# Optimization experiments

Measured on AMD Instinct MI355X. Metric: run time of the kernel, lower is better.

## Reference

```python
import jax, jax.numpy as jnp
import numpy as np

B, L, D, H, TOPO = 2, 1024, 1024, 16, 8
Dh = D // H
N_SLOTS = B * L


def _rope_apply(x, cos, sin):
    # x: [B,H,L,Dh]; cos/sin: [B,1,L,Dh//2]
    x1 = x[..., 0::2]
    x2 = x[..., 1::2]
    y1 = x1 * cos - x2 * sin
    y2 = x1 * sin + x2 * cos
    return jnp.stack([y1, y2], axis=-1).reshape(x.shape)


def setup_inputs() -> dict:
    key = jax.random.key(0)
    ks = jax.random.split(key, 6)
    x = jax.random.normal(ks[0], (B, L, D), dtype=jnp.float32)
    topo_active = jax.random.normal(ks[1], (B, L, TOPO), dtype=jnp.float32)
    k_cache = jnp.zeros((1, H, N_SLOTS, Dh), dtype=jnp.float32)
    v_cache = jnp.zeros((1, H, N_SLOTS, Dh), dtype=jnp.float32)
    Wqkv = jax.random.normal(ks[2], (3 * D, D), dtype=jnp.float32) * 0.02
    Wproj = jax.random.normal(ks[3], (D, D), dtype=jnp.float32) * 0.02
    Wfreq = jax.random.normal(ks[4], (Dh // 2, TOPO), dtype=jnp.float32) * 0.02
    # each token (b, pos) writes to physical slot b*L + pos
    slot_mapping = jnp.arange(N_SLOTS, dtype=jnp.int64)
    # paged causal mask: query (b, i) may see slot s iff slot belongs to batch b and pos(s) <= i
    s = jnp.arange(N_SLOTS)
    sb = s // L           # batch owning each slot
    sp = s % L            # position within that sequence
    b_idx = jnp.arange(B)[:, None, None]
    i_idx = jnp.arange(L)[None, :, None]
    block_mask = ((sb[None, None, :] == b_idx) & (sp[None, None, :] <= i_idx))[:, None]  # [B,1,L,S]
    return {"x": x, "topo_active": topo_active, "k_cache": k_cache, "v_cache": v_cache,
            "Wqkv": Wqkv, "Wproj": Wproj, "Wfreq": Wfreq,
            "slot_mapping": slot_mapping, "block_mask": block_mask}


def reference(x, topo_active, k_cache, v_cache, Wqkv, Wproj, Wfreq, slot_mapping, block_mask):
    Bx, Lx, Dx = x.shape
    # qkv projection -> q,k,v [B,H,L,Dh]
    qkv = (x @ Wqkv.T).reshape(Bx, Lx, 3, H, Dh).transpose(2, 0, 3, 1, 4)
    q, k, v = qkv[0], qkv[1], qkv[2]
    # RnRoPE: topo -> per-position frequencies, rotate q and k
    freqs = (topo_active @ Wfreq.T)[:, None]  # [B,1,L,Dh//2]
    cos, sin = jnp.cos(freqs), jnp.sin(freqs)
    q = _rope_apply(q, cos, sin)
    k = _rope_apply(k, cos, sin)
    # commit new k/v into the paged cache via slot_mapping scatter
    k_flat = k.transpose(0, 2, 1, 3).reshape(Bx * Lx, H, Dh).swapaxes(0, 1)  # [H,BL,Dh]
    v_flat = v.transpose(0, 2, 1, 3).reshape(Bx * Lx, H, Dh).swapaxes(0, 1)
    kc = k_cache[0].at[:, slot_mapping].set(k_flat)  # [H,S,Dh]
    vc = v_cache[0].at[:, slot_mapping].set(v_flat)
    # masked (block-sparse) attention over the physical cache
    scale = 1.0 / jnp.sqrt(jnp.float32(Dh))
    scores = jnp.einsum('bhld,hsd->bhls', q, kc) * scale
    scores = jnp.where(block_mask, scores, -jnp.inf)
    p = jax.nn.softmax(scores, axis=-1)
    out = jnp.einsum('bhls,hsd->bhld', p, vc)
    out = out.transpose(0, 2, 1, 3).reshape(Bx, Lx, Dx)
    return out @ Wproj.T
```

## Files before the change

kernel.cpp:

```cpp
#include <hip/hip_runtime.h>
#include <hip/hip_bf16.h>
#include <math.h>

#define H_N 16
#define DH 64
#define LSEQ 1024
#define BATCH 2
#define NSLOT 2048
#define DMODEL 1024

typedef __bf16 bf16x8 __attribute__((ext_vector_type(8)));
typedef __bf16 bf16x4 __attribute__((ext_vector_type(4)));
typedef float f32x4 __attribute__((ext_vector_type(4)));

__global__ __launch_bounds__(256) void k_setup(const float* __restrict__ x,
                                               const float* __restrict__ Wqkv,
                                               const float* __restrict__ Wproj,
                                               const float* __restrict__ topo,
                                               const float* __restrict__ Wfreq,
                                               __bf16* __restrict__ xb,
                                               __bf16* __restrict__ Wqkvb,
                                               __bf16* __restrict__ Wprojb,
                                               float* __restrict__ cosb,
                                               float* __restrict__ sinb) {
    int blk = blockIdx.x;
    if (blk < 6144) {
        const float* in;
        __bf16* out;
        int base;
        if (blk < 2048)      { in = x;     out = xb;     base = blk; }
        else if (blk < 5120) { in = Wqkv;  out = Wqkvb;  base = blk - 2048; }
        else                 { in = Wproj; out = Wprojb; base = blk - 5120; }
        int i = (base * 256 + threadIdx.x) * 4;
        float4 v = *reinterpret_cast<const float4*>(in + i);
        struct B4 { __bf16 a, b, c, d; };
        B4 o{(__bf16)v.x, (__bf16)v.y, (__bf16)v.z, (__bf16)v.w};
        *reinterpret_cast<B4*>(out + i) = o;
    } else {
        int s = (blk - 6144) * 8 + (threadIdx.x >> 5);
        int j = threadIdx.x & 31;
        float f = 0.f;
#pragma unroll
        for (int t = 0; t < 8; ++t) f += topo[s * 8 + t] * Wfreq[j * 8 + t];
        cosb[s * 32 + j] = cosf(f);
        sinb[s * 32 + j] = sinf(f);
    }
}

template <int BM, int BN, int BK>
__device__ __forceinline__ void gemm_coreT(const __bf16* __restrict__ A,
                                           const __bf16* __restrict__ Bm,
                                           int K, int m0, int n0,
                                           __bf16* As, __bf16* Bs,
                                           f32x4 acc[BM / 32][BN / 32],
                                           int tid, int wr, int wc, int lane) {
    constexpr int MF = BM / 32, NF = BN / 32;
    constexpr int SLOTS = BK / 8;
    constexpr int RPI = 256 / SLOTS;
    constexpr int AIT = BM / RPI;
    constexpr int BIT = BN / RPI;
    const f32x4 z = {0.f, 0.f, 0.f, 0.f};
#pragma unroll
    for (int m = 0; m < MF; ++m)
#pragma unroll
        for (int n = 0; n < NF; ++n) acc[m][n] = z;

    const int l15 = lane & 15, g = lane >> 4;
    const int wv = tid >> 6;
    const int srow = tid / SLOTS, sslot = tid % SLOTS;
    const int ssrc = (sslot ^ (srow & 7)) * 8;

#pragma unroll
    for (int i = 0; i < AIT; ++i) {
        int row = i * RPI + srow;
        __builtin_amdgcn_global_load_lds(
            (const __attribute__((address_space(1))) void*)(A + (size_t)(m0 + row) * K + ssrc),
            (__attribute__((address_space(3))) void*)(As + i * 2048 + wv * 512), 16, 0, 0);
    }
#pragma unroll
    for (int i = 0; i < BIT; ++i) {
        int row = i * RPI + srow;
        __builtin_amdgcn_global_load_lds(
            (const __attribute__((address_space(1))) void*)(Bm + (size_t)(n0 + row) * K + ssrc),
            (__attribute__((address_space(3))) void*)(Bs + i * 2048 + wv * 512), 16, 0, 0);
    }
    __syncthreads();

    const int NT = K / BK;
    for (int t = 0; t < NT; ++t) {
        const int cur = t & 1;
        __bf16* Ac = As + cur * (BM * BK);
        __bf16* Bc = Bs + cur * (BN * BK);
        if (t + 1 < NT) {
            const int k0 = (t + 1) * BK;
            __bf16* An = As + (1 - cur) * (BM * BK);
            __bf16* Bn = Bs + (1 - cur) * (BN * BK);
#pragma unroll
            for (int i = 0; i < AIT; ++i) {
                int row = i * RPI + srow;
                __builtin_amdgcn_global_load_lds(
                    (const __attribute__((address_space(1))) void*)(A + (size_t)(m0 + row) * K + k0 + ssrc),
                    (__attribute__((address_space(3))) void*)(An + i * 2048 + wv * 512), 16, 0, 0);
            }
#pragma unroll
            for (int i = 0; i < BIT; ++i) {
                int row = i * RPI + srow;
                __builtin_amdgcn_global_load_lds(
                    (const __attribute__((address_space(1))) void*)(Bm + (size_t)(n0 + row) * K + k0 + ssrc),
                    (__attribute__((address_space(3))) void*)(Bn + i * 2048 + wv * 512), 16, 0, 0);
            }
        }
        __builtin_amdgcn_s_setprio(1);
#pragma unroll
        for (int kk = 0; kk < BK / 32; ++kk) {
            const int k16 = kk * 4 + g;
            bf16x8 af[MF], bfr[NF];
#pragma unroll
            for (int m = 0; m < MF; ++m) {
                int row = wr * (BM / 2) + m * 16 + l15;
                int slot = k16 ^ (row & 7);
                af[m] = *reinterpret_cast<const bf16x8*>(Ac + row * BK + slot * 8);
            }
#pragma unroll
            for (int n = 0; n < NF; ++n) {
                int col = wc * (BN / 2) + n * 16 + l15;
                int slot = k16 ^ (col & 7);
                bfr[n] = *reinterpret_cast<const bf16x8*>(Bc + col * BK + slot * 8);
            }
#pragma unroll
            for (int m = 0; m < MF; ++m)
#pragma unroll
                for (int n = 0; n < NF; ++n)
                    acc[m][n] = __builtin_amdgcn_mfma_f32_16x16x32_bf16(af[m], bfr[n], acc[m][n], 0, 0, 0);
        }
        __builtin_amdgcn_s_setprio(0);
        __syncthreads();
    }
}

__global__ __launch_bounds__(256, 2) void k_qkv_mfma(const __bf16* __restrict__ xb,
                                                     const __bf16* __restrict__ Wb,
                                                     const float* __restrict__ cosb,
                                                     const float* __restrict__ sinb,
                                                     __bf16* __restrict__ Qb,
                                                     __bf16* __restrict__ Kb,
                                                     __bf16* __restrict__ Vtb) {
    __shared__ __bf16 As[2][128 * 64];
    __shared__ __bf16 Bs[2][96 * 64];
    int lin = blockIdx.x;
    int newlin = (lin & 7) * 64 + (lin >> 3);
    const int m0 = (newlin & 15) * 128, n0 = (newlin >> 4) * 96;
    const int tid = threadIdx.x, lane = tid & 63, w = tid >> 6;
    const int wr = w >> 1, wc = w & 1;
    const int l15 = lane & 15, g = lane >> 4;
    f32x4 acc[4][3];
    gemm_coreT<128, 96, 64>(xb, Wb, DMODEL, m0, n0, &As[0][0], &Bs[0][0], acc, tid, wr, wc, lane);

    const int rbase = m0 + wr * 64;
#pragma unroll
    for (int n = 0; n < 3; ++n) {
        int c = n0 + wc * 48 + n * 16 + l15;
        int part = c >> 10, h = (c >> 6) & 15, d = c & 63, jj = d >> 1;
#pragma unroll
        for (int m = 0; m < 4; ++m) {
            int sbase = rbase + m * 16 + g * 4;
            if (part < 2) {
                __bf16* dst = (part == 0) ? Qb : Kb;
#pragma unroll
                for (int j = 0; j < 4; ++j) {
                    int s = sbase + j;
                    float v = acc[m][n][j];
                    float partner = __shfl_xor(v, 1);
                    float cs = cosb[s * 32 + jj], sn = sinb[s * 32 + jj];
                    float outv = (d & 1) ? fmaf(v, cs, partner * sn) : fmaf(v, cs, -partner * sn);
                    dst[((size_t)h * NSLOT + s) * DH + d] = (__bf16)outv;
                }
            } else {
                bf16x4 pk;
#pragma unroll
                for (int j = 0; j < 4; ++j) pk[j] = (__bf16)acc[m][n][j];
                *reinterpret_cast<bf16x4*>(&Vtb[((size_t)h * DH + d) * NSLOT + sbase]) = pk;
            }
        }
    }
}

__global__ __launch_bounds__(256, 2) void k_attn9(const __bf16* __restrict__ Qg,
                                                  const __bf16* __restrict__ Kg,
                                                  const __bf16* __restrict__ Vt,
                                                  __bf16* __restrict__ AO) {
    int lin = blockIdx.x + 16 * (blockIdx.y + 16 * blockIdx.z);
    const int x = lin & 7;
    const int t = lin >> 3;
    const int b = x >> 2;
    const int h = (x & 3) * 4 + (t & 3);
    const int v = t >> 2;
    const int bx = (v < 8) ? v : 23 - v;

    const int tid = threadIdx.x, w = tid >> 6, lane = tid & 63;
    const int l15 = lane & 15, g = lane >> 4;
    const int q0 = bx * 64 + w * 16;

    __shared__ __bf16 Ks[2][128 * 64];
    __shared__ __bf16 Vs[2][64 * 128];
    __shared__ __bf16 P_lds[4][16 * 128];

    const __bf16* Qh = Qg + ((size_t)h * NSLOT + b * LSEQ) * DH;
    const __bf16* Kh = Kg + ((size_t)h * NSLOT + b * LSEQ) * DH;
    const __bf16* Vh = Vt + ((size_t)h * DH) * NSLOT + b * LSEQ;

    bf16x8 qf[2];
#pragma unroll
    for (int g2 = 0; g2 < 2; ++g2)
        qf[g2] = *reinterpret_cast<const bf16x8*>(Qh + (size_t)(q0 + l15) * DH + g2 * 32 + g * 8);

    const f32x4 z = {0.f, 0.f, 0.f, 0.f};
    f32x4 ao[4];
#pragma unroll
    for (int dt = 0; dt < 4; ++dt) ao[dt] = z;
    float lsum[4] = {0.f, 0.f, 0.f, 0.f};

    const int nch = (bx >> 1) + 1;

#pragma unroll
    for (int i = 0; i < 4; ++i) {
        int u = i * 256 + tid;
        {
            int row = u >> 3, slot = u & 7, srcs = (slot ^ (row & 7)) * 8;
            __builtin_amdgcn_global_load_lds(
                (const __attribute__((address_space(1))) void*)(Kh + (size_t)row * DH + srcs),
                (__attribute__((address_space(3))) void*)(&Ks[0][i * 2048 + (tid >> 6) * 512]), 16, 0, 0);
        }
        {
            int row = u >> 4, slot = u & 15, srcs = (slot ^ (row & 7)) * 8;
            __builtin_amdgcn_global_load_lds(
                (const __attribute__((address_space(1))) void*)(Vh + (size_t)row * NSLOT + srcs),
                (__attribute__((address_space(3))) void*)(&Vs[0][i * 2048 + (tid >> 6) * 512]), 16, 0, 0);
        }
    }
    __syncthreads();

    for (int ch = 0; ch < nch; ++ch) {
        const int cur = ch & 1;
        if (ch + 1 < nch) {
            const int nsp = (ch + 1) * 128;
#pragma unroll
            for (int i = 0; i < 4; ++i) {
                int u = i * 256 + tid;
                {
                    int row = u >> 3, slot = u & 7, srcs = (slot ^ (row & 7)) * 8;
                    __builtin_amdgcn_global_load_lds(
                        (const __attribute__((address_space(1))) void*)(Kh + (size_t)(nsp + row) * DH + srcs),
                        (__attribute__((address_space(3))) void*)(&Ks[1 - cur][i * 2048 + (tid >> 6) * 512]), 16, 0, 0);
                }
                {
                    int row = u >> 4, slot = u & 15, srcs = (slot ^ (row & 7)) * 8;
                    __builtin_amdgcn_global_load_lds(
                        (const __attribute__((address_space(1))) void*)(Vh + (size_t)row * NSLOT + nsp + srcs),
                        (__attribute__((address_space(3))) void*)(&Vs[1 - cur][i * 2048 + (tid >> 6) * 512]), 16, 0, 0);
                }
            }
        }

        f32x4 s[8];
#pragma unroll
        for (int n = 0; n < 8; ++n) s[n] = z;
        __builtin_amdgcn_s_setprio(1);
#pragma unroll
        for (int g2 = 0; g2 < 2; ++g2) {
#pragma unroll
            for (int n = 0; n < 8; ++n) {
                int r = n * 16 + l15;
                int slot = ((g2 << 2) + g) ^ (r & 7);
                bf16x8 kf = *reinterpret_cast<const bf16x8*>(&Ks[cur][r * 64 + slot * 8]);
                s[n] = __builtin_amdgcn_mfma_f32_16x16x32_bf16(qf[g2], kf, s[n], 0, 0, 0);
            }
        }
        __builtin_amdgcn_s_setprio(0);

        const bool last = (ch == nch - 1);
        const int sp0 = ch * 128;
#pragma unroll
        for (int n = 0; n < 8; ++n) {
            int key = sp0 + n * 16 + l15;
#pragma unroll
            for (int j = 0; j < 4; ++j) {
                float sc = s[n][j] * 0.125f;
                if (last && key > q0 + g * 4 + j) sc = -INFINITY;
                float p = __expf(sc);
                s[n][j] = p;
                lsum[j] += p;
            }
        }

#pragma unroll
        for (int j = 0; j < 4; ++j) {
            int row = g * 4 + j;
#pragma unroll
            for (int n = 0; n < 8; ++n) {
                int slot = n * 2 + (l15 >> 3);
                P_lds[w][row * 128 + ((slot ^ (row & 7)) << 3) + (l15 & 7)] = (__bf16)s[n][j];
            }
        }

        bf16x8 pf[4];
#pragma unroll
        for (int kb = 0; kb < 4; ++kb)
            pf[kb] = *reinterpret_cast<const bf16x8*>(
                &P_lds[w][l15 * 128 + (((kb << 2) + g) ^ (l15 & 7)) * 8]);

        __builtin_amdgcn_s_setprio(1);
#pragma unroll
        for (int kb = 0; kb < 4; ++kb) {
#pragma unroll
            for (int dt = 0; dt < 4; ++dt) {
                int rv = dt * 16 + l15;
                int slot = ((kb << 2) + g) ^ (rv & 7);
                bf16x8 vf = *reinterpret_cast<const bf16x8*>(&Vs[cur][rv * 128 + slot * 8]);
                ao[dt] = __builtin_amdgcn_mfma_f32_16x16x32_bf16(pf[kb], vf, ao[dt], 0, 0, 0);
            }
        }
        __builtin_amdgcn_s_setprio(0);

        __syncthreads();
    }

    float lrow[4];
#pragma unroll
    for (int j = 0; j < 4; ++j) {
        float vv = lsum[j];
#pragma unroll
        for (int off = 1; off < 16; off <<= 1) vv += __shfl_xor(vv, off);
        lrow[j] = vv;
    }

#pragma unroll
    for (int dt = 0; dt < 4; ++dt)
#pragma unroll
        for (int j = 0; j < 4; ++j) {
            int q = q0 + g * 4 + j;
            AO[(size_t)(b * LSEQ + q) * DMODEL + h * 64 + dt * 16 + l15] =
                (__bf16)(ao[dt][j] / lrow[j]);
        }
}

__global__ __launch_bounds__(256, 2) void k_proj_mfma(const __bf16* __restrict__ AO,
                                                      const __bf16* __restrict__ Wb,
                                                      float* __restrict__ out) {
    __shared__ __bf16 As[2][64 * 128];
    __shared__ __bf16 Bs[2][64 * 128];
    int lin = blockIdx.x;
    int newlin = (lin & 7) * 64 + (lin >> 3);
    const int m0 = (newlin & 31) * 64, n0 = (newlin >> 5) * 64;
    const int tid = threadIdx.x, lane = tid & 63, w = tid >> 6;
    const int wr = w >> 1, wc = w & 1;
    const int l15 = lane & 15, g = lane >> 4;
    f32x4 acc[2][2];
    gemm_coreT<64, 64, 128>(AO, Wb, DMODEL, m0, n0, &As[0][0], &Bs[0][0], acc, tid, wr, wc, lane);

#pragma unroll
    for (int n = 0; n < 2; ++n) {
        int c = n0 + wc * 32 + n * 16 + l15;
#pragma unroll
        for (int m = 0; m < 2; ++m) {
#pragma unroll
            for (int j = 0; j < 4; ++j) {
                int s = m0 + wr * 32 + m * 16 + g * 4 + j;
                out[(size_t)s * DMODEL + c] = acc[m][n][j];
            }
        }
    }
}

extern "C" void kernel_launch(void* const* d_in, const int* in_sizes, int n_in,
                              void* d_out, int out_size, void* d_ws, size_t ws_size,
                              hipStream_t stream) {
    const float* x     = (const float*)d_in[0];
    const float* topo  = (const float*)d_in[1];
    const float* Wqkv  = (const float*)d_in[4];
    const float* Wproj = (const float*)d_in[5];
    const float* Wfreq = (const float*)d_in[6];
    float* out = (float*)d_out;

    char* wsb = (char*)d_ws;
    __bf16* xb     = (__bf16*)(wsb + 0);
    __bf16* Wqkvb  = (__bf16*)(wsb + (4u << 20));
    __bf16* Wprojb = (__bf16*)(wsb + (10u << 20));
    float*  cosb   = (float*)(wsb + (12u << 20));
    float*  sinb   = (float*)(wsb + (12u << 20) + 262144);
    __bf16* Qb     = (__bf16*)(wsb + (12u << 20) + 524288);
    __bf16* Kb     = (__bf16*)(wsb + (16u << 20) + 524288);
    __bf16* Vtb    = (__bf16*)(wsb + (20u << 20) + 524288);
    __bf16* AO     = (__bf16*)(wsb + (24u << 20) + 524288);

    hipLaunchKernelGGL(k_setup, dim3(6400), dim3(256), 0, stream,
                       x, Wqkv, Wproj, topo, Wfreq, xb, Wqkvb, Wprojb, cosb, sinb);
    hipLaunchKernelGGL(k_qkv_mfma, dim3(512), dim3(256), 0, stream,
                       xb, Wqkvb, cosb, sinb, Qb, Kb, Vtb);
    hipLaunchKernelGGL(k_attn9, dim3(LSEQ / 64, H_N, BATCH), dim3(256), 0, stream,
                       Qb, Kb, Vtb, AO);
    hipLaunchKernelGGL(k_proj_mfma, dim3(512), dim3(256), 0, stream,
                       AO, Wprojb, out);
}
```

Measured before the change: 62.54 us.

## Fuse all four stages into one cooperative persistent kernel with grid syncs

Merges the setup, QKV GEMM with RoPE, attention and projection kernels into a single cooperative kernel of 512 blocks, separated by grid-wide syncs. The goal is to remove the launch gaps and tail effects between the four separate launches. The fused attention phase loses double-buffered K/V prefetch and now loads each chunk synchronously, which adds memory latency. Grid syncs and a single fixed 64KB shared-memory allocation may also limit occupancy; the old multi-kernel path is kept as a fallback.

```diff
diff --git a/kernel.cpp b/kernel.cpp
--- a/kernel.cpp
+++ b/kernel.cpp
@@ -1,6 +1,9 @@
 #include <hip/hip_runtime.h>
 #include <hip/hip_bf16.h>
+#include <hip/hip_cooperative_groups.h>
 #include <math.h>
+
+namespace cg = cooperative_groups;
 
 #define H_N 16
 #define DH 64
@@ -12,40 +15,6 @@
 typedef __bf16 bf16x8 __attribute__((ext_vector_type(8)));
 typedef __bf16 bf16x4 __attribute__((ext_vector_type(4)));
 typedef float f32x4 __attribute__((ext_vector_type(4)));
-
-__global__ __launch_bounds__(256) void k_setup(const float* __restrict__ x,
-                                               const float* __restrict__ Wqkv,
-                                               const float* __restrict__ Wproj,
-                                               const float* __restrict__ topo,
-                                               const float* __restrict__ Wfreq,
-                                               __bf16* __restrict__ xb,
-                                               __bf16* __restrict__ Wqkvb,
-                                               __bf16* __restrict__ Wprojb,
-                                               float* __restrict__ cosb,
-                                               float* __restrict__ sinb) {
-    int blk = blockIdx.x;
-    if (blk < 6144) {
-        const float* in;
-        __bf16* out;
-        int base;
-        if (blk < 2048)      { in = x;     out = xb;     base = blk; }
-        else if (blk < 5120) { in = Wqkv;  out = Wqkvb;  base = blk - 2048; }
-        else                 { in = Wproj; out = Wprojb; base = blk - 5120; }
-        int i = (base * 256 + threadIdx.x) * 4;
-        float4 v = *reinterpret_cast<const float4*>(in + i);
-        struct B4 { __bf16 a, b, c, d; };
-        B4 o{(__bf16)v.x, (__bf16)v.y, (__bf16)v.z, (__bf16)v.w};
-        *reinterpret_cast<B4*>(out + i) = o;
-    } else {
-        int s = (blk - 6144) * 8 + (threadIdx.x >> 5);
-        int j = threadIdx.x & 31;
-        float f = 0.f;
-#pragma unroll
-        for (int t = 0; t < 8; ++t) f += topo[s * 8 + t] * Wfreq[j * 8 + t];
-        cosb[s * 32 + j] = cosf(f);
-        sinb[s * 32 + j] = sinf(f);
-    }
-}
 
 template <int BM, int BN, int BK>
 __device__ __forceinline__ void gemm_coreT(const __bf16* __restrict__ A,
@@ -136,6 +105,284 @@
         __builtin_amdgcn_s_setprio(0);
         __syncthreads();
     }
+}
+
+__device__ __forceinline__ void setup_body(int blk, int tid,
+                                           const float* x, const float* Wqkv, const float* Wproj,
+                                           const float* topo, const float* Wfreq,
+                                           __bf16* xb, __bf16* Wqkvb, __bf16* Wprojb,
+                                           float* cosb, float* sinb) {
+    if (blk < 6144) {
+        const float* in;
+        __bf16* ob;
+        int base;
+        if (blk < 2048)      { in = x;     ob = xb;     base = blk; }
+        else if (blk < 5120) { in = Wqkv;  ob = Wqkvb;  base = blk - 2048; }
+        else                 { in = Wproj; ob = Wprojb; base = blk - 5120; }
+        int i = (base * 256 + tid) * 4;
+        float4 v = *reinterpret_cast<const float4*>(in + i);
+        struct B4 { __bf16 a, b, c, d; };
+        B4 o{(__bf16)v.x, (__bf16)v.y, (__bf16)v.z, (__bf16)v.w};
+        *reinterpret_cast<B4*>(ob + i) = o;
+    } else {
+        int s = (blk - 6144) * 8 + (tid >> 5);
+        int j = tid & 31;
+        float f = 0.f;
+#pragma unroll
+        for (int t = 0; t < 8; ++t) f += topo[s * 8 + t] * Wfreq[j * 8 + t];
+        cosb[s * 32 + j] = cosf(f);
+        sinb[s * 32 + j] = sinf(f);
+    }
+}
+
+__device__ __forceinline__ void qkv_epilogue(f32x4 acc[4][3], int m0, int n0,
+                                             int wr, int wc, int l15, int g,
+                                             const float* cosb, const float* sinb,
+                                             __bf16* Qb, __bf16* Kb, __bf16* Vtb) {
+    const int rbase = m0 + wr * 64;
+#pragma unroll
+    for (int n = 0; n < 3; ++n) {
+        int c = n0 + wc * 48 + n * 16 + l15;
+        int part = c >> 10, h = (c >> 6) & 15, d = c & 63, jj = d >> 1;
+#pragma unroll
+        for (int m = 0; m < 4; ++m) {
+            int sbase = rbase + m * 16 + g * 4;
+            if (part < 2) {
+                __bf16* dst = (part == 0) ? Qb : Kb;
+#pragma unroll
+                for (int j = 0; j < 4; ++j) {
+                    int s = sbase + j;
+                    float v = acc[m][n][j];
+                    float partner = __shfl_xor(v, 1);
+                    float cs = cosb[s * 32 + jj], sn = sinb[s * 32 + jj];
+                    float outv = (d & 1) ? fmaf(v, cs, partner * sn) : fmaf(v, cs, -partner * sn);
+                    dst[((size_t)h * NSLOT + s) * DH + d] = (__bf16)outv;
+                }
+            } else {
+                bf16x4 pk;
+#pragma unroll
+                for (int j = 0; j < 4; ++j) pk[j] = (__bf16)acc[m][n][j];
+                *reinterpret_cast<bf16x4*>(&Vtb[((size_t)h * DH + d) * NSLOT + sbase]) = pk;
+            }
+        }
+    }
+}
+
+__device__ __forceinline__ void attn_chunk(const bf16x8 qf[2], __bf16* Kc, __bf16* Vc,
+                                           __bf16* Pw, int ch, int nch, int q0,
+                                           int l15, int g, f32x4 ao[4], float lsum[4]) {
+    const f32x4 z = {0.f, 0.f, 0.f, 0.f};
+    f32x4 s[8];
+#pragma unroll
+    for (int n = 0; n < 8; ++n) s[n] = z;
+    __builtin_amdgcn_s_setprio(1);
+#pragma unroll
+    for (int g2 = 0; g2 < 2; ++g2) {
+#pragma unroll
+        for (int n = 0; n < 8; ++n) {
+            int r = n * 16 + l15;
+            int slot = ((g2 << 2) + g) ^ (r & 7);
+            bf16x8 kf = *reinterpret_cast<const bf16x8*>(Kc + r * 64 + slot * 8);
+            s[n] = __builtin_amdgcn_mfma_f32_16x16x32_bf16(qf[g2], kf, s[n], 0, 0, 0);
+        }
+    }
+    __builtin_amdgcn_s_setprio(0);
+
+    const bool last = (ch == nch - 1);
+    const int sp0 = ch * 128;
+#pragma unroll
+    for (int n = 0; n < 8; ++n) {
+        int key = sp0 + n * 16 + l15;
+#pragma unroll
+        for (int j = 0; j < 4; ++j) {
+            float sc = s[n][j] * 0.125f;
+            if (last && key > q0 + g * 4 + j) sc = -INFINITY;
+            float p = __expf(sc);
+            s[n][j] = p;
+            lsum[j] += p;
+        }
+    }
+
+#pragma unroll
+    for (int j = 0; j < 4; ++j) {
+        int row = g * 4 + j;
+#pragma unroll
+        for (int n = 0; n < 8; ++n) {
+            int slot = n * 2 + (l15 >> 3);
+            Pw[row * 128 + ((slot ^ (row & 7)) << 3) + (l15 & 7)] = (__bf16)s[n][j];
+        }
+    }
+
+    bf16x8 pf[4];
+#pragma unroll
+    for (int kb = 0; kb < 4; ++kb)
+        pf[kb] = *reinterpret_cast<const bf16x8*>(
+            Pw + l15 * 128 + (((kb << 2) + g) ^ (l15 & 7)) * 8);
+
+    __builtin_amdgcn_s_setprio(1);
+#pragma unroll
+    for (int kb = 0; kb < 4; ++kb) {
+#pragma unroll
+        for (int dt = 0; dt < 4; ++dt) {
+            int rv = dt * 16 + l15;
+            int slot = ((kb << 2) + g) ^ (rv & 7);
+            bf16x8 vf = *reinterpret_cast<const bf16x8*>(Vc + rv * 128 + slot * 8);
+            ao[dt] = __builtin_amdgcn_mfma_f32_16x16x32_bf16(pf[kb], vf, ao[dt], 0, 0, 0);
+        }
+    }
+    __builtin_amdgcn_s_setprio(0);
+}
+
+__global__ __launch_bounds__(256, 2) void k_fused(const float* __restrict__ x,
+                                                  const float* __restrict__ topo,
+                                                  const float* __restrict__ Wqkv,
+                                                  const float* __restrict__ Wproj,
+                                                  const float* __restrict__ Wfreq,
+                                                  float* __restrict__ out,
+                                                  char* __restrict__ wsb) {
+    __shared__ __align__(16) char smem[65536];
+
+    __bf16* xb     = (__bf16*)(wsb);
+    __bf16* Wqkvb  = (__bf16*)(wsb + (4u << 20));
+    __bf16* Wprojb = (__bf16*)(wsb + (10u << 20));
+    float*  cosb   = (float*)(wsb + (12u << 20));
+    float*  sinb   = (float*)(wsb + (12u << 20) + 262144);
+    __bf16* Qb     = (__bf16*)(wsb + (12u << 20) + 524288);
+    __bf16* Kb     = (__bf16*)(wsb + (16u << 20) + 524288);
+    __bf16* Vtb    = (__bf16*)(wsb + (20u << 20) + 524288);
+    __bf16* AO     = (__bf16*)(wsb + (24u << 20) + 524288);
+
+    cg::grid_group grid = cg::this_grid();
+    const int tid = threadIdx.x;
+    const int bid = blockIdx.x;
+    const int lane = tid & 63, w = tid >> 6;
+    const int l15 = lane & 15, g = lane >> 4;
+
+    for (int blk = bid; blk < 6400; blk += 512)
+        setup_body(blk, tid, x, Wqkv, Wproj, topo, Wfreq, xb, Wqkvb, Wprojb, cosb, sinb);
+    grid.sync();
+
+    {
+        __bf16* As = (__bf16*)smem;
+        __bf16* Bs = (__bf16*)(smem + 32768);
+        int newlin = (bid & 7) * 64 + (bid >> 3);
+        const int m0 = (newlin & 15) * 128, n0 = (newlin >> 4) * 96;
+        const int wr = w >> 1, wc = w & 1;
+        f32x4 acc[4][3];
+        gemm_coreT<128, 96, 64>(xb, Wqkvb, DMODEL, m0, n0, As, Bs, acc, tid, wr, wc, lane);
+        qkv_epilogue(acc, m0, n0, wr, wc, l15, g, cosb, sinb, Qb, Kb, Vtb);
+    }
+    grid.sync();
+
+    {
+        __bf16* Ks = (__bf16*)smem;
+        __bf16* Vs = (__bf16*)(smem + 16384);
+        __bf16* Pw = (__bf16*)(smem + 32768) + w * 16 * 128;
+
+        const int xc = bid & 7;
+        const int t = bid >> 3;
+        const int b = xc >> 2;
+        const int h = (xc & 3) * 4 + (t & 3);
+        const int v = t >> 2;
+        const int bx = (v < 8) ? v : 23 - v;
+        const int q0 = bx * 64 + w * 16;
+
+        const __bf16* Qh = Qb + ((size_t)h * NSLOT + b * LSEQ) * DH;
+        const __bf16* Kh = Kb + ((size_t)h * NSLOT + b * LSEQ) * DH;
+        const __bf16* Vh = Vtb + ((size_t)h * DH) * NSLOT + b * LSEQ;
+
+        bf16x8 qf[2];
+#pragma unroll
+        for (int g2 = 0; g2 < 2; ++g2)
+            qf[g2] = *reinterpret_cast<const bf16x8*>(Qh + (size_t)(q0 + l15) * DH + g2 * 32 + g * 8);
+
+        const f32x4 z = {0.f, 0.f, 0.f, 0.f};
+        f32x4 ao[4];
+#pragma unroll
+        for (int dt = 0; dt < 4; ++dt) ao[dt] = z;
+        float lsum[4] = {0.f, 0.f, 0.f, 0.f};
+
+        const int nch = (bx >> 1) + 1;
+
+        for (int ch = 0; ch < nch; ++ch) {
+            __syncthreads();
+            const int sp0 = ch * 128;
+#pragma unroll
+            for (int i = 0; i < 4; ++i) {
+                int u = i * 256 + tid;
+                {
+                    int row = u >> 3, slot = u & 7, srcs = (slot ^ (row & 7)) * 8;
+                    __builtin_amdgcn_global_load_lds(
+                        (const __attribute__((address_space(1))) void*)(Kh + (size_t)(sp0 + row) * DH + srcs),
+                        (__attribute__((address_space(3))) void*)(Ks + i * 2048 + w * 512), 16, 0, 0);
+                }
+                {
+                    int row = u >> 4, slot = u & 15, srcs = (slot ^ (row & 7)) * 8;
+                    __builtin_amdgcn_global_load_lds(
+                        (const __attribute__((address_space(1))) void*)(Vh + (size_t)row * NSLOT + sp0 + srcs),
+                        (__attribute__((address_space(3))) void*)(Vs + i * 2048 + w * 512), 16, 0, 0);
+                }
+            }
+            __syncthreads();
+            attn_chunk(qf, Ks, Vs, Pw, ch, nch, q0, l15, g, ao, lsum);
+        }
+
+        float lrow[4];
+#pragma unroll
+        for (int j = 0; j < 4; ++j) {
+            float vv = lsum[j];
+#pragma unroll
+            for (int off = 1; off < 16; off <<= 1) vv += __shfl_xor(vv, off);
+            lrow[j] = vv;
+        }
+
+#pragma unroll
+        for (int dt = 0; dt < 4; ++dt)
+#pragma unroll
+            for (int j = 0; j < 4; ++j) {
+                int q = q0 + g * 4 + j;
+                AO[(size_t)(b * LSEQ + q) * DMODEL + h * 64 + dt * 16 + l15] =
+                    (__bf16)(ao[dt][j] / lrow[j]);
+            }
+    }
+    grid.sync();
+
+    {
+        __bf16* As = (__bf16*)smem;
+        __bf16* Bs = (__bf16*)(smem + 32768);
+        int newlin = (bid & 7) * 64 + (bid >> 3);
+        const int m0 = (newlin & 31) * 64, n0 = (newlin >> 5) * 64;
+        const int wr = w >> 1, wc = w & 1;
+        f32x4 acc[2][2];
+        gemm_coreT<64, 64, 128>(AO, Wprojb, DMODEL, m0, n0, As, Bs, acc, tid, wr, wc, lane);
+
+#pragma unroll
+        for (int n = 0; n < 2; ++n) {
+            int c = n0 + wc * 32 + n * 16 + l15;
+#pragma unroll
+            for (int m = 0; m < 2; ++m) {
+#pragma unroll
+                for (int j = 0; j < 4; ++j) {
+                    int s = m0 + wr * 32 + m * 16 + g * 4 + j;
+                    out[(size_t)s * DMODEL + c] = acc[m][n][j];
+                }
+            }
+        }
+    }
+}
+
+__global__ __launch_bounds__(256) void k_setup(const float* __restrict__ x,
+                                               const float* __restrict__ Wqkv,
+                                               const float* __restrict__ Wproj,
+                                               const float* __restrict__ topo,
+                                               const float* __restrict__ Wfreq,
+                                               __bf16* __restrict__ xb,
+                                               __bf16* __restrict__ Wqkvb,
+                                               __bf16* __restrict__ Wprojb,
+                                               float* __restrict__ cosb,
+                                               float* __restrict__ sinb) {
+    setup_body(blockIdx.x, threadIdx.x, x, Wqkv, Wproj, topo, Wfreq,
+               xb, Wqkvb, Wprojb, cosb, sinb);
 }
 
 __global__ __launch_bounds__(256, 2) void k_qkv_mfma(const __bf16* __restrict__ xb,
@@ -155,34 +402,7 @@
     const int l15 = lane & 15, g = lane >> 4;
     f32x4 acc[4][3];
     gemm_coreT<128, 96, 64>(xb, Wb, DMODEL, m0, n0, &As[0][0], &Bs[0][0], acc, tid, wr, wc, lane);
-
-    const int rbase = m0 + wr * 64;
-#pragma unroll
-    for (int n = 0; n < 3; ++n) {
-        int c = n0 + wc * 48 + n * 16 + l15;
-        int part = c >> 10, h = (c >> 6) & 15, d = c & 63, jj = d >> 1;
-#pragma unroll
-        for (int m = 0; m < 4; ++m) {
-            int sbase = rbase + m * 16 + g * 4;
-            if (part < 2) {
-                __bf16* dst = (part == 0) ? Qb : Kb;
-#pragma unroll
-                for (int j = 0; j < 4; ++j) {
-                    int s = sbase + j;
-                    float v = acc[m][n][j];
-                    float partner = __shfl_xor(v, 1);
-                    float cs = cosb[s * 32 + jj], sn = sinb[s * 32 + jj];
-                    float outv = (d & 1) ? fmaf(v, cs, partner * sn) : fmaf(v, cs, -partner * sn);
-                    dst[((size_t)h * NSLOT + s) * DH + d] = (__bf16)outv;
-                }
-            } else {
-                bf16x4 pk;
-#pragma unroll
-                for (int j = 0; j < 4; ++j) pk[j] = (__bf16)acc[m][n][j];
-                *reinterpret_cast<bf16x4*>(&Vtb[((size_t)h * DH + d) * NSLOT + sbase]) = pk;
-            }
-        }
-    }
+    qkv_epilogue(acc, m0, n0, wr, wc, l15, g, cosb, sinb, Qb, Kb, Vtb);
 }
 
 __global__ __launch_bounds__(256, 2) void k_attn9(const __bf16* __restrict__ Qg,
@@ -190,10 +410,10 @@
                                                   const __bf16* __restrict__ Vt,
                                                   __bf16* __restrict__ AO) {
     int lin = blockIdx.x + 16 * (blockIdx.y + 16 * blockIdx.z);
-    const int x = lin & 7;
+    const int xc = lin & 7;
     const int t = lin >> 3;
-    const int b = x >> 2;
-    const int h = (x & 3) * 4 + (t & 3);
+    const int b = xc >> 2;
+    const int h = (xc & 3) * 4 + (t & 3);
     const int v = t >> 2;
     const int bx = (v < 8) ? v : 23 - v;
 
@@ -204,6 +424,7 @@
     __shared__ __bf16 Ks[2][128 * 64];
     __shared__ __bf16 Vs[2][64 * 128];
     __shared__ __bf16 P_lds[4][16 * 128];
+    __bf16* Pw = &P_lds[w][0];
 
     const __bf16* Qh = Qg + ((size_t)h * NSLOT + b * LSEQ) * DH;
     const __bf16* Kh = Kg + ((size_t)h * NSLOT + b * LSEQ) * DH;
@@ -229,13 +450,13 @@
             int row = u >> 3, slot = u & 7, srcs = (slot ^ (row & 7)) * 8;
             __builtin_amdgcn_global_load_lds(
                 (const __attribute__((address_space(1))) void*)(Kh + (size_t)row * DH + srcs),
-                (__attribute__((address_space(3))) void*)(&Ks[0][i * 2048 + (tid >> 6) * 512]), 16, 0, 0);
+                (__attribute__((address_space(3))) void*)(&Ks[0][i * 2048 + w * 512]), 16, 0, 0);
         }
         {
             int row = u >> 4, slot = u & 15, srcs = (slot ^ (row & 7)) * 8;
             __builtin_amdgcn_global_load_lds(
                 (const __attribute__((address_space(1))) void*)(Vh + (size_t)row * NSLOT + srcs),
-                (__attribute__((address_space(3))) void*)(&Vs[0][i * 2048 + (tid >> 6) * 512]), 16, 0, 0);
+                (__attribute__((address_space(3))) void*)(&Vs[0][i * 2048 + w * 512]), 16, 0, 0);
         }
     }
     __syncthreads();
@@ -251,77 +472,17 @@
                     int row = u >> 3, slot = u & 7, srcs = (slot ^ (row & 7)) * 8;
                     __builtin_amdgcn_global_load_lds(
                         (const __attribute__((address_space(1))) void*)(Kh + (size_t)(nsp + row) * DH + srcs),
-                        (__attribute__((address_space(3))) void*)(&Ks[1 - cur][i * 2048 + (tid >> 6) * 512]), 16, 0, 0);
+                        (__attribute__((address_space(3))) void*)(&Ks[1 - cur][i * 2048 + w * 512]), 16, 0, 0);
                 }
                 {
                     int row = u >> 4, slot = u & 15, srcs = (slot ^ (row & 7)) * 8;
                     __builtin_amdgcn_global_load_lds(
                         (const __attribute__((address_space(1))) void*)(Vh + (size_t)row * NSLOT + nsp + srcs),
-                        (__attribute__((address_space(3))) void*)(&Vs[1 - cur][i * 2048 + (tid >> 6) * 512]), 16, 0, 0);
+                        (__attribute__((address_space(3))) void*)(&Vs[1 - cur][i * 2048 + w * 512]), 16, 0, 0);
                 }
             }
         }
-
-        f32x4 s[8];
-#pragma unroll
-        for (int n = 0; n < 8; ++n) s[n] = z;
-        __builtin_amdgcn_s_setprio(1);
-#pragma unroll
-        for (int g2 = 0; g2 < 2; ++g2) {
-#pragma unroll
-            for (int n = 0; n < 8; ++n) {
-                int r = n * 16 + l15;
-                int slot = ((g2 << 2) + g) ^ (r & 7);
-                bf16x8 kf = *reinterpret_cast<const bf16x8*>(&Ks[cur][r * 64 + slot * 8]);
-                s[n] = __builtin_amdgcn_mfma_f32_16x16x32_bf16(qf[g2], kf, s[n], 0, 0, 0);
-            }
-        }
-        __builtin_amdgcn_s_setprio(0);
-
-        const bool last = (ch == nch - 1);
-        const int sp0 = ch * 128;
-#pragma unroll
-        for (int n = 0; n < 8; ++n) {
-            int key = sp0 + n * 16 + l15;
-#pragma unroll
-            for (int j = 0; j < 4; ++j) {
-                float sc = s[n][j] * 0.125f;
-                if (last && key > q0 + g * 4 + j) sc = -INFINITY;
-                float p = __expf(sc);
-                s[n][j] = p;
-                lsum[j] += p;
-            }
-        }
-
-#pragma unroll
-        for (int j = 0; j < 4; ++j) {
-            int row = g * 4 + j;
-#pragma unroll
-            for (int n = 0; n < 8; ++n) {
-                int slot = n * 2 + (l15 >> 3);
-                P_lds[w][row * 128 + ((slot ^ (row & 7)) << 3) + (l15 & 7)] = (__bf16)s[n][j];
-            }
-        }
-
-        bf16x8 pf[4];
-#pragma unroll
-        for (int kb = 0; kb < 4; ++kb)
-            pf[kb] = *reinterpret_cast<const bf16x8*>(
-                &P_lds[w][l15 * 128 + (((kb << 2) + g) ^ (l15 & 7)) * 8]);
-
-        __builtin_amdgcn_s_setprio(1);
-#pragma unroll
-        for (int kb = 0; kb < 4; ++kb) {
-#pragma unroll
-            for (int dt = 0; dt < 4; ++dt) {
-                int rv = dt * 16 + l15;
-                int slot = ((kb << 2) + g) ^ (rv & 7);
-                bf16x8 vf = *reinterpret_cast<const bf16x8*>(&Vs[cur][rv * 128 + slot * 8]);
-                ao[dt] = __builtin_amdgcn_mfma_f32_16x16x32_bf16(pf[kb], vf, ao[dt], 0, 0, 0);
-            }
-        }
-        __builtin_amdgcn_s_setprio(0);
-
+        attn_chunk(qf, &Ks[cur][0], &Vs[cur][0], Pw, ch, nch, q0, l15, g, ao, lsum);
         __syncthreads();
     }
 
@@ -381,9 +542,22 @@
     const float* Wproj = (const float*)d_in[5];
     const float* Wfreq = (const float*)d_in[6];
     float* out = (float*)d_out;
-
     char* wsb = (char*)d_ws;
-    __bf16* xb     = (__bf16*)(wsb + 0);
+
+    int coopAttr = 0, dev = 0, nb = 0;
+    hipGetDevice(&dev);
+    hipDeviceGetAttribute(&coopAttr, hipDeviceAttributeCooperativeLaunch, dev);
+    hipOccupancyMaxActiveBlocksPerMultiprocessor(&nb, (const void*)k_fused, 256, 0);
+
+    if (coopAttr && nb >= 2) {
+        void* args[] = {(void*)&x, (void*)&topo, (void*)&Wqkv, (void*)&Wproj,
+                        (void*)&Wfreq, (void*)&out, (void*)&wsb};
+        hipLaunchCooperativeKernel((const void*)k_fused, dim3(512), dim3(256),
+                                   args, 0, stream);
+        return;
+    }
+
+    __bf16* xb     = (__bf16*)(wsb);
     __bf16* Wqkvb  = (__bf16*)(wsb + (4u << 20));
     __bf16* Wprojb = (__bf16*)(wsb + (10u << 20));
     float*  cosb   = (float*)(wsb + (12u << 20));
```

Measured after the change: 61.37 us. No clear change (-1.9%).
